# Kernel optimization log

Hardware: AMD Instinct MI355X
Metric: run time of the kernel (lower is better)

## Reference

```python
import jax, jax.numpy as jnp
import numpy as np

B, S, HID = 2, 2048, 2048
NH, HD = 16, 128
KVC, QC = 512, 1536


def _rope(x):
    # x: [B, H, S, D]; interleaved-pair rotation matching the torch view(..., D//2, 2)
    b, h, s, d = x.shape
    inv_freq = 1.0 / (10000.0 ** (jnp.arange(0, d, 2, dtype=jnp.float32) / d))  # [D/2]
    pos = jnp.arange(s, dtype=jnp.float32)
    sinusoid = pos[:, None] * inv_freq[None, :]  # [S, D/2]
    sin = jnp.sin(sinusoid)[None, None]  # [1,1,S,D/2]
    cos = jnp.cos(sinusoid)[None, None]
    xr = x.reshape(b, h, s, d // 2, 2)
    x1, x2 = xr[..., 0], xr[..., 1]
    out = jnp.stack([x1 * cos - x2 * sin, x1 * sin + x2 * cos], axis=-1)
    return out.reshape(b, h, s, d)


def setup_inputs() -> dict:
    key = jax.random.key(0)
    ks = jax.random.split(key, 14)
    def lin(k, fan_in, fan_out):
        lim = 1.0 / np.sqrt(fan_in)
        kw, kb = jax.random.split(k)
        W = jax.random.uniform(kw, (fan_in, fan_out), jnp.float32, -lim, lim)
        b = jax.random.uniform(kb, (fan_out,), jnp.float32, -lim, lim)
        return W, b
    x = jax.random.normal(ks[0], (B, S, HID), jnp.float32)
    # causal mask (positions with 0 are masked out)
    attention_mask = jnp.tril(jnp.ones((S, S), jnp.int32))[None, None]  # [1,1,S,S]
    W_dkv, b_dkv = lin(ks[1], HID, KVC)
    W_uk, b_uk = lin(ks[2], KVC, NH * HD)
    W_uv, b_uv = lin(ks[3], KVC, NH * HD)
    W_dq, b_dq = lin(ks[4], HID, QC)
    W_uq, b_uq = lin(ks[5], QC, NH * HD)
    W_o, b_o = lin(ks[6], NH * HD, HID)
    return dict(x=x, attention_mask=attention_mask,
                W_dkv=W_dkv, b_dkv=b_dkv, W_uk=W_uk, b_uk=b_uk,
                W_uv=W_uv, b_uv=b_uv, W_dq=W_dq, b_dq=b_dq,
                W_uq=W_uq, b_uq=b_uq, W_o=W_o, b_o=b_o)


def reference(x, attention_mask, W_dkv, b_dkv, W_uk, b_uk, W_uv, b_uv,
              W_dq, b_dq, W_uq, b_uq, W_o, b_o):
    b, s, _ = x.shape
    kv = x @ W_dkv + b_dkv                                   # [B,S,KVC]
    k = (kv @ W_uk + b_uk).reshape(b, s, NH, HD).transpose(0, 2, 1, 3)  # [B,H,S,D]
    v = (kv @ W_uv + b_uv).reshape(b, s, NH, HD).transpose(0, 2, 1, 3)
    q = ((x @ W_dq + b_dq) @ W_uq + b_uq).reshape(b, s, NH, HD).transpose(0, 2, 1, 3)
    q, k = _rope(q), _rope(k)
    scores = jnp.einsum('bhqd,bhkd->bhqk', q, k) / jnp.sqrt(jnp.float32(HD))
    scores = jnp.where(attention_mask == 0, jnp.float32(-1e9), scores)
    probs = jax.nn.softmax(scores, axis=-1)
    out = jnp.einsum('bhqk,bhkd->bhqd', probs, v)            # [B,H,S,D]
    out = out.transpose(0, 2, 1, 3).reshape(b, s, NH * HD)
    return out @ W_o + b_o
```

## Files before the change

### kernel.cpp

```cpp
#include <hip/hip_runtime.h>
#include <stdint.h>

typedef unsigned short u16;
typedef uint32_t u32;
typedef __attribute__((ext_vector_type(8))) short short8;
typedef __attribute__((ext_vector_type(4))) float f32x4;
typedef __attribute__((ext_vector_type(4))) u32 u32x4;
typedef __attribute__((ext_vector_type(2))) u32 u32x2;
typedef __attribute__((ext_vector_type(4))) unsigned short u16x4;

#define BS_ 4096
#define S_ 2048
#define HID_ 2048

__device__ __forceinline__ float bf2f(u16 u) { union { u32 i; float f; } v; v.i = ((u32)u) << 16; return v.f; }
__device__ __forceinline__ u16 f2bf(float f) {
  union { float f; u32 i; } v; v.f = f;
  u32 r = v.i + 0x7fffu + ((v.i >> 16) & 1u);
  return (u16)(r >> 16);
}

__device__ __forceinline__ void gload16(const void* gsrc, void* ldst) {
  __builtin_amdgcn_global_load_lds(
      (const __attribute__((address_space(1))) void*)gsrc,
      (__attribute__((address_space(3))) void*)ldst, 16, 0, 0);
}

__global__ __launch_bounds__(256) void prep(const float* __restrict__ x, u16* __restrict__ xb,
                                            const float* __restrict__ W_dkv, const float* __restrict__ W_dq,
                                            const float* __restrict__ W_uk, const float* __restrict__ W_uv,
                                            const float* __restrict__ W_uq, const float* __restrict__ W_o,
                                            u16* __restrict__ WdkvqT, u16* __restrict__ WukvT,
                                            u16* __restrict__ WuqT, u16* __restrict__ WoT,
                                            const float* __restrict__ b_dkv, const float* __restrict__ b_dq,
                                            const float* __restrict__ b_uk, const float* __restrict__ b_uv,
                                            float* __restrict__ cs, float* __restrict__ bc1,
                                            float* __restrict__ bc2) {
  __shared__ float tile[64][65];
  int b = blockIdx.x;
  const int t = threadIdx.x;
  if (b < 8192) {
    int i = b * 256 + t;
    float4 v = ((const float4*)x)[i];
    u16x4 o;
    o.x = f2bf(v.x); o.y = f2bf(v.y); o.z = f2bf(v.z); o.w = f2bf(v.w);
    ((u16x4*)xb)[i] = o;
    return;
  }
  b -= 8192;
  if (b < 3328) {
    const float* W; u16* WT; int K, N, gx, r = b;
    if (r < 256)                 { W = W_dkv; WT = WdkvqT;                    K = 2048; N = 512;  gx = 8;  }
    else if ((r -= 256) < 768)   { W = W_dq;  WT = WdkvqT + (size_t)512 * 2048; K = 2048; N = 1536; gx = 24; }
    else if ((r -= 768) < 256)   { W = W_uk;  WT = WukvT;                     K = 512;  N = 2048; gx = 32; }
    else if ((r -= 256) < 256)   { W = W_uv;  WT = WukvT + (size_t)2048 * 512;  K = 512;  N = 2048; gx = 32; }
    else if ((r -= 256) < 768)   { W = W_uq;  WT = WuqT;                      K = 1536; N = 2048; gx = 32; }
    else                         { r -= 768;  W = W_o; WT = WoT;              K = 2048; N = 2048; gx = 32; }
    const int nb = (r % gx) * 64, kb = (r / gx) * 64;
#pragma unroll
    for (int c = 0; c < 4; ++c) {
      int idx = c * 256 + t;
      int row = idx >> 4;
      int col4 = (idx & 15) * 4;
      float4 v = *(const float4*)&W[(size_t)(kb + row) * N + nb + col4];
      tile[row][col4 + 0] = v.x; tile[row][col4 + 1] = v.y;
      tile[row][col4 + 2] = v.z; tile[row][col4 + 3] = v.w;
    }
    __syncthreads();
#pragma unroll
    for (int c = 0; c < 4; ++c) {
      int idx = c * 256 + t;
      int n = idx >> 4;
      int k4 = (idx & 15) * 4;
      u16x4 o;
      o.x = f2bf(tile[k4 + 0][n]); o.y = f2bf(tile[k4 + 1][n]);
      o.z = f2bf(tile[k4 + 2][n]); o.w = f2bf(tile[k4 + 3][n]);
      *(u16x4*)&WT[(size_t)(nb + n) * K + kb + k4] = o;
    }
    return;
  }
  b -= 3328;
  if (b < 512) {
    int idx = b * 256 + t;
    int pos = idx >> 6, i = idx & 63;
    float inv = powf(10000.f, -(float)i / 64.f);
    float a = (float)pos * inv;
    cs[idx * 2] = cosf(a);
    cs[idx * 2 + 1] = sinf(a);
    return;
  }
  b -= 512;
  {
    int i = b * 256 + t;
    if (i < 512) bc1[i] = b_dkv[i];
    else if (i < 2048) bc1[i] = b_dq[i - 512];
    else if (i < 4096) bc2[i - 2048] = b_uk[i - 2048];
    else if (i < 6144) bc2[i - 2048] = b_uv[i - 4096];
  }
}

template <int OUTF32>
__global__ __launch_bounds__(256) void gemm_bt(const u16* __restrict__ A, int lda,
                                               const u16* __restrict__ BT,
                                               const float* __restrict__ bias,
                                               void* __restrict__ Cout,
                                               int M, int N, int K) {
  __shared__ u16 As[2][128 * 64];
  __shared__ u16 Bs[2][128 * 64];
  const int t = threadIdx.x;
  const int lane = t & 63, wave = t >> 6;
  const int wm = wave >> 1, wn = wave & 1;
  const int gx = gridDim.x;
  const int nwg = gx * gridDim.y;
  const int flat = blockIdx.y * gx + blockIdx.x;
  const int swz = (flat & 7) * (nwg >> 3) + (flat >> 3);
  const int tn = swz % gx, tm = swz / gx;
  const int r16 = lane & 15, q4 = lane >> 4;

  f32x4 acc[4][4];
#pragma unroll
  for (int m = 0; m < 4; ++m)
#pragma unroll
    for (int n = 0; n < 4; ++n) acc[m][n] = (f32x4){0.f, 0.f, 0.f, 0.f};

  auto stg = [&](int bufi, int kt) {
#pragma unroll
    for (int c = 0; c < 4; ++c) {
      int idx = c * 256 + t;
      int row = idx >> 3, ch = idx & 7;
      gload16(&A[(size_t)(tm * 128 + row) * lda + kt + ch * 8], (char*)As[bufi] + idx * 16);
      gload16(&BT[(size_t)(tn * 128 + row) * K + kt + ch * 8], (char*)Bs[bufi] + idx * 16);
    }
  };

  const int nkt = K >> 6;
  stg(0, 0);
  __syncthreads();
  for (int it = 0; it < nkt; ++it) {
    const int buf = it & 1;
    if (it + 1 < nkt) stg(buf ^ 1, (it + 1) << 6);
#pragma unroll
    for (int kk = 0; kk < 64; kk += 32) {
      short8 af[4], bfv[4];
#pragma unroll
      for (int m = 0; m < 4; ++m)
        af[m] = *(const short8*)&As[buf][(wm * 64 + m * 16 + r16) * 64 + kk + q4 * 8];
#pragma unroll
      for (int n = 0; n < 4; ++n)
        bfv[n] = *(const short8*)&Bs[buf][(wn * 64 + n * 16 + r16) * 64 + kk + q4 * 8];
      __builtin_amdgcn_s_setprio(1);
#pragma unroll
      for (int m = 0; m < 4; ++m)
#pragma unroll
        for (int n = 0; n < 4; ++n)
          acc[m][n] = __builtin_amdgcn_mfma_f32_16x16x32_bf16(bfv[n], af[m], acc[m][n], 0, 0, 0);
      __builtin_amdgcn_s_setprio(0);
    }
    __syncthreads();
  }
#pragma unroll
  for (int n = 0; n < 4; ++n) {
    int gc0 = tn * 128 + wn * 64 + n * 16 + q4 * 4;
    float4 bv4 = *(const float4*)&bias[gc0];
#pragma unroll
    for (int m = 0; m < 4; ++m) {
      int grow = tm * 128 + wm * 64 + m * 16 + r16;
      float v0 = acc[m][n][0] + bv4.x, v1 = acc[m][n][1] + bv4.y;
      float v2 = acc[m][n][2] + bv4.z, v3 = acc[m][n][3] + bv4.w;
      if (OUTF32) {
        float4 o; o.x = v0; o.y = v1; o.z = v2; o.w = v3;
        *(float4*)&((float*)Cout)[(size_t)grow * N + gc0] = o;
      } else {
        u16x4 o; o.x = f2bf(v0); o.y = f2bf(v1); o.z = f2bf(v2); o.w = f2bf(v3);
        *(u16x4*)&((u16*)Cout)[(size_t)grow * N + gc0] = o;
      }
    }
  }
}

__global__ __launch_bounds__(256) void gemm23(const u16* __restrict__ kvq1,
                                              const u16* __restrict__ WukvT, const u16* __restrict__ WuqT,
                                              const float* __restrict__ bc2, const float* __restrict__ b_uq,
                                              const float* __restrict__ cs,
                                              u16* __restrict__ kbuf, u16* __restrict__ VT,
                                              u16* __restrict__ qb) {
  __shared__ u16 sh[4 * 128 * 64];
  const int t = threadIdx.x;
  const int lane = t & 63, wave = t >> 6;
  const int wm = wave >> 1, wn = wave & 1;
  const int bflat = blockIdx.x;
  const bool g2 = (bflat >= 512);
  const u16* A  = g2 ? kvq1 : (kvq1 + 512);
  const u16* BT = g2 ? WukvT : WuqT;
  const float* bias = g2 ? bc2 : b_uq;
  const int K = g2 ? 512 : 1536;
  const int gx = g2 ? 32 : 16;
  const int nwg = g2 ? 1024 : 512;
  const int flat = g2 ? (bflat - 512) : bflat;
  const int swz = (flat & 7) * (nwg >> 3) + (flat >> 3);
  const int tn = swz % gx, tm = swz / gx;
  const int r16 = lane & 15, q4 = lane >> 4;

  f32x4 acc[4][4];
#pragma unroll
  for (int m = 0; m < 4; ++m)
#pragma unroll
    for (int n = 0; n < 4; ++n) acc[m][n] = (f32x4){0.f, 0.f, 0.f, 0.f};

  auto stg = [&](int bufi, int kt) {
    char* Asb = (char*)(sh + bufi * 16384);
    char* Bsb = Asb + 16384;
#pragma unroll
    for (int c = 0; c < 4; ++c) {
      int idx = c * 256 + t;
      int row = idx >> 3, ch = idx & 7;
      gload16(&A[(size_t)(tm * 128 + row) * 2048 + kt + ch * 8], Asb + idx * 16);
      gload16(&BT[(size_t)(tn * 128 + row) * K + kt + ch * 8], Bsb + idx * 16);
    }
  };

  const int nkt = K >> 6;
  stg(0, 0);
  __syncthreads();
  for (int it = 0; it < nkt; ++it) {
    const int buf = it & 1;
    if (it + 1 < nkt) stg(buf ^ 1, (it + 1) << 6);
    const u16* As = sh + buf * 16384;
    const u16* Bs = As + 8192;
#pragma unroll
    for (int kk = 0; kk < 64; kk += 32) {
      short8 af[4], bfv[4];
#pragma unroll
      for (int m = 0; m < 4; ++m)
        af[m] = *(const short8*)&As[(wm * 64 + m * 16 + r16) * 64 + kk + q4 * 8];
#pragma unroll
      for (int n = 0; n < 4; ++n)
        bfv[n] = *(const short8*)&Bs[(wn * 64 + n * 16 + r16) * 64 + kk + q4 * 8];
      __builtin_amdgcn_s_setprio(1);
#pragma unroll
      for (int m = 0; m < 4; ++m)
#pragma unroll
        for (int n = 0; n < 4; ++n)
          acc[m][n] = __builtin_amdgcn_mfma_f32_16x16x32_bf16(bfv[n], af[m], acc[m][n], 0, 0, 0);
      __builtin_amdgcn_s_setprio(0);
    }
    __syncthreads();
  }

  const bool isV = g2 && (tn >= 16);
  if (!isV) {
    u16* outp = g2 ? kbuf : qb;
#pragma unroll
    for (int n = 0; n < 4; ++n) {
      int gc0 = tn * 128 + wn * 64 + n * 16 + q4 * 4;
      float4 bv4 = *(const float4*)&bias[gc0];
      const int i0 = (gc0 & 127) >> 1;
#pragma unroll
      for (int m = 0; m < 4; ++m) {
        int grow = tm * 128 + wm * 64 + m * 16 + r16;
        float v0 = acc[m][n][0] + bv4.x, v1 = acc[m][n][1] + bv4.y;
        float v2 = acc[m][n][2] + bv4.z, v3 = acc[m][n][3] + bv4.w;
        int s = grow & 2047;
        float4 cp = *(const float4*)&cs[((size_t)s * 64 + i0) * 2];
        float y0 = v0 * cp.x - v1 * cp.y;
        float y1 = v0 * cp.y + v1 * cp.x;
        float y2 = v2 * cp.z - v3 * cp.w;
        float y3 = v2 * cp.w + v3 * cp.z;
        u16x4 o; o.x = f2bf(y0); o.y = f2bf(y1); o.z = f2bf(y2); o.w = f2bf(y3);
        *(u16x4*)&outp[(size_t)grow * 2048 + gc0] = o;
      }
    }
  } else {
    u16* lt = sh;
    __syncthreads();
#pragma unroll
    for (int n = 0; n < 4; ++n) {
      int gc0 = tn * 128 + wn * 64 + n * 16 + q4 * 4;
      float4 bv4 = *(const float4*)&bias[gc0];
      int dL0 = wn * 64 + n * 16 + q4 * 4;
#pragma unroll
      for (int m = 0; m < 4; ++m) {
        int sL = wm * 64 + m * 16 + r16;
        float vv[4] = {acc[m][n][0] + bv4.x, acc[m][n][1] + bv4.y,
                       acc[m][n][2] + bv4.z, acc[m][n][3] + bv4.w};
#pragma unroll
        for (int j = 0; j < 4; ++j) {
          int dd = dL0 + j;
          lt[dd * 128 + (sL ^ ((dd & 7) << 4))] = f2bf(vv[j]);
        }
      }
    }
    __syncthreads();
    const int hh = tn - 16;
    const int bb2 = tm >> 4;
    const int s0 = (tm & 15) * 128;
    u16* vbase = VT + (size_t)(bb2 * 16 + hh) * 128 * S_ + s0;
#pragma unroll
    for (int c = 0; c < 8; ++c) {
      int idx = c * 256 + t;
      int d = idx >> 4, ch = idx & 15;
      short8 v = *(const short8*)&lt[d * 128 + ((ch * 8) ^ ((d & 7) << 4))];
      *(short8*)&vbase[(size_t)d * S_ + ch * 8] = v;
    }
  }
}

__global__ __launch_bounds__(256, 2) void attn_kernel(const u16* __restrict__ Q, const u16* __restrict__ K,
                                                      int kld, const u16* __restrict__ VT,
                                                      u16* __restrict__ O) {
  __shared__ char smem[75776];
  u16* Kl = (u16*)smem;
  u16* Vl = (u16*)(smem + 32768);
  u16* Pl = (u16*)(smem + 65536);
  float* ex = (float*)smem;

  const int t = threadIdx.x;
  const int lane = t & 63, w = t >> 6;
  const int r16 = lane & 15, q4 = lane >> 4;
  const int par = w >> 1, sub = w & 1;
  const int b = blockIdx.x;
  const int xcd = b & 7, u = b >> 3;
  const int p = u & 15, g4 = u >> 4;
  const int bh = g4 * 8 + xcd;
  const int bb = bh >> 4, h = bh & 15;
  const u16* Qb = Q + (size_t)bb * S_ * HID_ + (size_t)h * 128;
  const u16* Kb = K + (size_t)bb * S_ * kld + (size_t)h * 128;
  const u16* VTb = VT + (size_t)bh * 128 * S_;
  u16* Ob = O + (size_t)bb * S_ * HID_ + (size_t)h * 128;

  auto stage = [&](int rs, int kvbase) {
#pragma unroll
    for (int pp = 0; pp < 2; ++pp) {
      int kvb = kvbase + pp * 32;
      char* kd = (char*)(Kl + (size_t)(rs * 2 + pp) * 4096);
      char* vd = (char*)(Vl + (size_t)(rs * 2 + pp) * 4096);
#pragma unroll
      for (int c = 0; c < 2; ++c) {
        int s = c * 256 + t;
        int row = s >> 4;
        int ch = (s & 15) ^ (row & 7);
        gload16(&Kb[(size_t)(kvb + row) * kld + ch * 8], kd + s * 16);
      }
#pragma unroll
      for (int c = 0; c < 2; ++c) {
        int s = c * 256 + t;
        int row = s >> 2;
        int ch = (s & 3) ^ ((row >> 1) & 3);
        gload16(&VTb[(size_t)row * S_ + kvb + ch * 8], vd + s * 16);
      }
    }
  };

  u16* Pw = Pl + (size_t)w * 1280;
  const float SCALE = 0.08838834764831845f;

#pragma unroll
  for (int seg = 0; seg < 2; ++seg) {
    const int qt = seg ? (31 - p) : p;
    const int nr = qt + 1;
    const int qrow0 = qt * 64 + sub * 32;

    short8 qf[2][4];
#pragma unroll
    for (int m = 0; m < 2; ++m)
#pragma unroll
      for (int dk = 0; dk < 4; ++dk)
        qf[m][dk] = *(const short8*)&Qb[(size_t)(qrow0 + m * 16 + r16) * HID_ + dk * 32 + q4 * 8];

    f32x4 ao[2][8];
    float mr[2], lr[2];
#pragma unroll
    for (int m = 0; m < 2; ++m) {
#pragma unroll
      for (int dn = 0; dn < 8; ++dn) ao[m][dn] = (f32x4){0.f, 0.f, 0.f, 0.f};
      mr[m] = -1e30f; lr[m] = 0.f;
    }

    stage(0, 0);
    __syncthreads();

    for (int r = 0; r < nr; ++r) {
      const int rs = r & 1;
      if (r + 1 < nr) stage(rs ^ 1, (r + 1) * 64);
      const int kv0 = r * 64 + par * 32;
      const u16* Kbuf = Kl + (size_t)(rs * 2 + par) * 4096;
      const u16* Vbuf = Vl + (size_t)(rs * 2 + par) * 4096;

      if (kv0 <= qrow0 + 31) {
        f32x4 sc[2][2];
#pragma unroll
        for (int m = 0; m < 2; ++m)
#pragma unroll
          for (int n = 0; n < 2; ++n) sc[m][n] = (f32x4){0.f, 0.f, 0.f, 0.f};
#pragma unroll
        for (int dk = 0; dk < 4; ++dk) {
          short8 kf[2];
#pragma unroll
          for (int n = 0; n < 2; ++n) {
            int kr = n * 16 + r16;
            int ba = (kr * 256 + dk * 64 + q4 * 16) ^ ((kr & 7) << 4);
            kf[n] = *(const short8*)((const char*)Kbuf + ba);
          }
          __builtin_amdgcn_s_setprio(1);
#pragma unroll
          for (int n = 0; n < 2; ++n)
#pragma unroll
            for (int m = 0; m < 2; ++m)
              sc[m][n] = __builtin_amdgcn_mfma_f32_16x16x32_bf16(kf[n], qf[m][dk], sc[m][n], 0, 0, 0);
          __builtin_amdgcn_s_setprio(0);
        }
        const bool nm = (kv0 + 31 > qrow0);
#pragma unroll
        for (int m = 0; m < 2; ++m) {
          const int q = qrow0 + m * 16 + r16;
#pragma unroll
          for (int n = 0; n < 2; ++n)
#pragma unroll
            for (int j = 0; j < 4; ++j) {
              float sv = sc[m][n][j] * SCALE;
              if (nm) {
                int kv = kv0 + n * 16 + q4 * 4 + j;
                if (kv > q) sv = -1e30f;
              }
              sc[m][n][j] = sv;
            }
        }
        float tm0[2];
#pragma unroll
        for (int m = 0; m < 2; ++m) {
          float tm = sc[m][0][0];
#pragma unroll
          for (int n = 0; n < 2; ++n)
#pragma unroll
            for (int j = 0; j < 4; ++j) tm = fmaxf(tm, sc[m][n][j]);
          tm = fmaxf(tm, __shfl_xor(tm, 16));
          tm = fmaxf(tm, __shfl_xor(tm, 32));
          tm0[m] = tm;
        }
        float growth = fmaxf(tm0[0] - mr[0], tm0[1] - mr[1]);
        if (!__all(growth <= 8.0f)) {
#pragma unroll
          for (int m = 0; m < 2; ++m) {
            float mnew = fmaxf(mr[m], tm0[m]);
            float fsc = __expf(mr[m] - mnew);
            lr[m] *= fsc; mr[m] = mnew;
#pragma unroll
            for (int dn = 0; dn < 8; ++dn) ao[m][dn] *= fsc;
          }
        }
#pragma unroll
        for (int m = 0; m < 2; ++m) {
          float ps = 0.f;
#pragma unroll
          for (int n = 0; n < 2; ++n)
#pragma unroll
            for (int j = 0; j < 4; ++j) {
              float pv = __expf(sc[m][n][j] - mr[m]);
              sc[m][n][j] = pv;
              ps += pv;
            }
          ps += __shfl_xor(ps, 16);
          ps += __shfl_xor(ps, 32);
          lr[m] += ps;
        }
#pragma unroll
        for (int m = 0; m < 2; ++m)
#pragma unroll
          for (int n = 0; n < 2; ++n) {
            u32 lo, hi;
            asm("v_cvt_pk_bf16_f32 %0, %1, %2" : "=v"(lo) : "v"(sc[m][n][0]), "v"(sc[m][n][1]));
            asm("v_cvt_pk_bf16_f32 %0, %1, %2" : "=v"(hi) : "v"(sc[m][n][2]), "v"(sc[m][n][3]));
            u32x2 pr; pr.x = lo; pr.y = hi;
            int ba = (m * 16 + r16) * 80 + n * 32 + q4 * 8;
            *(u32x2*)((char*)Pw + ba) = pr;
          }
        short8 pb[2];
#pragma unroll
        for (int m = 0; m < 2; ++m)
          pb[m] = *(const short8*)((const char*)Pw + (m * 16 + r16) * 80 + q4 * 16);
        __builtin_amdgcn_s_setprio(1);
#pragma unroll
        for (int dn = 0; dn < 8; ++dn) {
          int d = dn * 16 + r16;
          int bv = d * 64 + ((q4 ^ ((d >> 1) & 3)) * 16);
          short8 vf = *(const short8*)((const char*)Vbuf + bv);
#pragma unroll
          for (int m = 0; m < 2; ++m)
            ao[m][dn] = __builtin_amdgcn_mfma_f32_16x16x32_bf16(vf, pb[m], ao[m][dn], 0, 0, 0);
        }
        __builtin_amdgcn_s_setprio(0);
      }
      __syncthreads();
    }

    {
      float* exb = ex + (size_t)sub * 4352 + (size_t)lane * 68;
      if (par == 1) {
#pragma unroll
        for (int m = 0; m < 2; ++m)
#pragma unroll
          for (int dn = 0; dn < 8; ++dn)
            *(f32x4*)(exb + m * 32 + dn * 4) = ao[m][dn];
        exb[64] = mr[0]; exb[65] = mr[1]; exb[66] = lr[0]; exb[67] = lr[1];
      }
      __syncthreads();
      if (par == 0) {
#pragma unroll
        for (int m = 0; m < 2; ++m) {
          float mB = exb[64 + m], lB = exb[66 + m];
          float mx = fmaxf(mr[m], mB);
          float wA = __expf(mr[m] - mx), wB = __expf(mB - mx);
          float inv = 1.f / (lr[m] * wA + lB * wB);
          const int q = qrow0 + m * 16 + r16;
#pragma unroll
          for (int dn = 0; dn < 8; ++dn) {
            f32x4 ob = *(const f32x4*)(exb + m * 32 + dn * 4);
            u16x4 o;
#pragma unroll
            for (int j = 0; j < 4; ++j) o[j] = f2bf((ao[m][dn][j] * wA + ob[j] * wB) * inv);
            *(u16x4*)&Ob[(size_t)q * HID_ + dn * 16 + q4 * 4] = o;
          }
        }
      }
      __syncthreads();
    }
  }
}

extern "C" void kernel_launch(void* const* d_in, const int* in_sizes, int n_in,
                              void* d_out, int out_size, void* d_ws, size_t ws_size,
                              hipStream_t stream) {
  (void)in_sizes; (void)n_in; (void)out_size; (void)ws_size;
  const float* x     = (const float*)d_in[0];
  const float* W_dkv = (const float*)d_in[2];
  const float* b_dkv = (const float*)d_in[3];
  const float* W_uk  = (const float*)d_in[4];
  const float* b_uk  = (const float*)d_in[5];
  const float* W_uv  = (const float*)d_in[6];
  const float* b_uv  = (const float*)d_in[7];
  const float* W_dq  = (const float*)d_in[8];
  const float* b_dq  = (const float*)d_in[9];
  const float* W_uq  = (const float*)d_in[10];
  const float* b_uq  = (const float*)d_in[11];
  const float* W_o   = (const float*)d_in[12];
  const float* b_o   = (const float*)d_in[13];
  float* out = (float*)d_out;

  char* ws = (char*)d_ws;
  size_t off = 0;
  auto carve = [&](size_t bytes) { void* p = ws + off; off += (bytes + 255) & ~(size_t)255; return p; };
  u16* xb     = (u16*)carve((size_t)BS_ * 2048 * 2);
  u16* WdkvqT = (u16*)carve((size_t)2048 * 2048 * 2);
  u16* WukvT  = (u16*)carve((size_t)4096 * 512 * 2);
  u16* WuqT   = (u16*)carve((size_t)2048 * 1536 * 2);
  u16* WoT    = (u16*)carve((size_t)2048 * 2048 * 2);
  u16* kvq1   = (u16*)carve((size_t)BS_ * 2048 * 2);
  u16* kbuf   = (u16*)carve((size_t)BS_ * 2048 * 2);
  u16* qb     = (u16*)carve((size_t)BS_ * 2048 * 2);
  u16* aob    = (u16*)carve((size_t)BS_ * 2048 * 2);
  float* cs   = (float*)carve((size_t)2048 * 64 * 2 * 4);
  float* bc1  = (float*)carve((size_t)2048 * 4);
  float* bc2  = (float*)carve((size_t)4096 * 4);
  u16* VT     = xb;

  prep<<<dim3(12056), 256, 0, stream>>>(x, xb, W_dkv, W_dq, W_uk, W_uv, W_uq, W_o,
                                        WdkvqT, WukvT, WuqT, WoT,
                                        b_dkv, b_dq, b_uk, b_uv, cs, bc1, bc2);

  gemm_bt<0><<<dim3(2048 / 128, BS_ / 128), 256, 0, stream>>>(xb, 2048, WdkvqT, bc1, kvq1, BS_, 2048, 2048);

  gemm23<<<dim3(1536), 256, 0, stream>>>(kvq1, WukvT, WuqT, bc2, b_uq, cs, kbuf, VT, qb);

  attn_kernel<<<dim3(512), 256, 0, stream>>>(qb, kbuf, 2048, VT, aob);

  gemm_bt<1><<<dim3(2048 / 128, BS_ / 128), 256, 0, stream>>>(aob, 2048, WoT, b_o, out, BS_, 2048, 2048);
}
```

Measured before the change: 258.9 us.

## Read V directly from global, shrink LDS, one q-tile per block for occupancy

Drops LDS staging of V in the attention kernel and loads V fragments straight from global memory into registers each iteration. This cuts shared memory from about 74KB to 42KB and raises launch bounds to 3 blocks per CU. The kernel also stops processing two paired q-tiles per block: it launches 1024 blocks with one q-tile each, heaviest tiles first, and splits the final merge into two smaller passes to fit the reduced LDS. The trade-off is uncoalesced, unpipelined global V reads and more register pressure from holding 8 V fragments, in exchange for higher occupancy and finer load balancing.

```diff
diff --git a/kernel.cpp b/kernel.cpp
--- a/kernel.cpp
+++ b/kernel.cpp
@@ -305,13 +305,12 @@
   }
 }
 
-__global__ __launch_bounds__(256, 2) void attn_kernel(const u16* __restrict__ Q, const u16* __restrict__ K,
+__global__ __launch_bounds__(256, 3) void attn_kernel(const u16* __restrict__ Q, const u16* __restrict__ K,
                                                       int kld, const u16* __restrict__ VT,
                                                       u16* __restrict__ O) {
-  __shared__ char smem[75776];
+  __shared__ char smem[43008];
   u16* Kl = (u16*)smem;
-  u16* Vl = (u16*)(smem + 32768);
-  u16* Pl = (u16*)(smem + 65536);
+  u16* Pl = (u16*)(smem + 32768);
   float* ex = (float*)smem;
 
   const int t = threadIdx.x;
@@ -319,21 +318,20 @@
   const int r16 = lane & 15, q4 = lane >> 4;
   const int par = w >> 1, sub = w & 1;
   const int b = blockIdx.x;
-  const int xcd = b & 7, u = b >> 3;
-  const int p = u & 15, g4 = u >> 4;
-  const int bh = g4 * 8 + xcd;
+  const int xcd = b & 7, i = (b >> 3) & 31, g = b >> 8;
+  const int qt = 31 - i;
+  const int bh = g * 8 + xcd;
   const int bb = bh >> 4, h = bh & 15;
   const u16* Qb = Q + (size_t)bb * S_ * HID_ + (size_t)h * 128;
   const u16* Kb = K + (size_t)bb * S_ * kld + (size_t)h * 128;
   const u16* VTb = VT + (size_t)bh * 128 * S_;
   u16* Ob = O + (size_t)bb * S_ * HID_ + (size_t)h * 128;
 
-  auto stage = [&](int rs, int kvbase) {
+  auto stageK = [&](int rs, int kvbase) {
 #pragma unroll
     for (int pp = 0; pp < 2; ++pp) {
       int kvb = kvbase + pp * 32;
       char* kd = (char*)(Kl + (size_t)(rs * 2 + pp) * 4096);
-      char* vd = (char*)(Vl + (size_t)(rs * 2 + pp) * 4096);
 #pragma unroll
       for (int c = 0; c < 2; ++c) {
         int s = c * 256 + t;
@@ -341,189 +339,173 @@
         int ch = (s & 15) ^ (row & 7);
         gload16(&Kb[(size_t)(kvb + row) * kld + ch * 8], kd + s * 16);
       }
-#pragma unroll
-      for (int c = 0; c < 2; ++c) {
-        int s = c * 256 + t;
-        int row = s >> 2;
-        int ch = (s & 3) ^ ((row >> 1) & 3);
-        gload16(&VTb[(size_t)row * S_ + kvb + ch * 8], vd + s * 16);
-      }
     }
   };
 
   u16* Pw = Pl + (size_t)w * 1280;
   const float SCALE = 0.08838834764831845f;
 
-#pragma unroll
-  for (int seg = 0; seg < 2; ++seg) {
-    const int qt = seg ? (31 - p) : p;
-    const int nr = qt + 1;
-    const int qrow0 = qt * 64 + sub * 32;
-
-    short8 qf[2][4];
-#pragma unroll
-    for (int m = 0; m < 2; ++m)
-#pragma unroll
-      for (int dk = 0; dk < 4; ++dk)
-        qf[m][dk] = *(const short8*)&Qb[(size_t)(qrow0 + m * 16 + r16) * HID_ + dk * 32 + q4 * 8];
-
-    f32x4 ao[2][8];
-    float mr[2], lr[2];
-#pragma unroll
-    for (int m = 0; m < 2; ++m) {
-#pragma unroll
-      for (int dn = 0; dn < 8; ++dn) ao[m][dn] = (f32x4){0.f, 0.f, 0.f, 0.f};
-      mr[m] = -1e30f; lr[m] = 0.f;
-    }
-
-    stage(0, 0);
-    __syncthreads();
-
-    for (int r = 0; r < nr; ++r) {
-      const int rs = r & 1;
-      if (r + 1 < nr) stage(rs ^ 1, (r + 1) * 64);
-      const int kv0 = r * 64 + par * 32;
-      const u16* Kbuf = Kl + (size_t)(rs * 2 + par) * 4096;
-      const u16* Vbuf = Vl + (size_t)(rs * 2 + par) * 4096;
-
-      if (kv0 <= qrow0 + 31) {
-        f32x4 sc[2][2];
+  const int nr = qt + 1;
+  const int qrow0 = qt * 64 + sub * 32;
+
+  short8 qf[2][4];
+#pragma unroll
+  for (int m = 0; m < 2; ++m)
+#pragma unroll
+    for (int dk = 0; dk < 4; ++dk)
+      qf[m][dk] = *(const short8*)&Qb[(size_t)(qrow0 + m * 16 + r16) * HID_ + dk * 32 + q4 * 8];
+
+  f32x4 ao[2][8];
+  float mr[2], lr[2];
+#pragma unroll
+  for (int m = 0; m < 2; ++m) {
+#pragma unroll
+    for (int dn = 0; dn < 8; ++dn) ao[m][dn] = (f32x4){0.f, 0.f, 0.f, 0.f};
+    mr[m] = -1e30f; lr[m] = 0.f;
+  }
+
+  stageK(0, 0);
+  __syncthreads();
+
+  for (int r = 0; r < nr; ++r) {
+    const int rs = r & 1;
+    if (r + 1 < nr) stageK(rs ^ 1, (r + 1) * 64);
+    const int kv0 = r * 64 + par * 32;
+    const u16* Kbuf = Kl + (size_t)(rs * 2 + par) * 4096;
+
+    if (kv0 <= qrow0 + 31) {
+      short8 vf[8];
+#pragma unroll
+      for (int dn = 0; dn < 8; ++dn)
+        vf[dn] = *(const short8*)&VTb[(size_t)(dn * 16 + r16) * S_ + kv0 + q4 * 8];
+      f32x4 sc[2][2];
+#pragma unroll
+      for (int m = 0; m < 2; ++m)
+#pragma unroll
+        for (int n = 0; n < 2; ++n) sc[m][n] = (f32x4){0.f, 0.f, 0.f, 0.f};
+#pragma unroll
+      for (int dk = 0; dk < 4; ++dk) {
+        short8 kf[2];
+#pragma unroll
+        for (int n = 0; n < 2; ++n) {
+          int kr = n * 16 + r16;
+          int ba = (kr * 256 + dk * 64 + q4 * 16) ^ ((kr & 7) << 4);
+          kf[n] = *(const short8*)((const char*)Kbuf + ba);
+        }
+        __builtin_amdgcn_s_setprio(1);
+#pragma unroll
+        for (int n = 0; n < 2; ++n)
+#pragma unroll
+          for (int m = 0; m < 2; ++m)
+            sc[m][n] = __builtin_amdgcn_mfma_f32_16x16x32_bf16(kf[n], qf[m][dk], sc[m][n], 0, 0, 0);
+        __builtin_amdgcn_s_setprio(0);
+      }
+      const bool nm = (kv0 + 31 > qrow0);
+#pragma unroll
+      for (int m = 0; m < 2; ++m) {
+        const int q = qrow0 + m * 16 + r16;
+#pragma unroll
+        for (int n = 0; n < 2; ++n)
+#pragma unroll
+          for (int j = 0; j < 4; ++j) {
+            float sv = sc[m][n][j] * SCALE;
+            if (nm) {
+              int kv = kv0 + n * 16 + q4 * 4 + j;
+              if (kv > q) sv = -1e30f;
+            }
+            sc[m][n][j] = sv;
+          }
+      }
+      float tm0[2];
+#pragma unroll
+      for (int m = 0; m < 2; ++m) {
+        float tm = sc[m][0][0];
+#pragma unroll
+        for (int n = 0; n < 2; ++n)
+#pragma unroll
+          for (int j = 0; j < 4; ++j) tm = fmaxf(tm, sc[m][n][j]);
+        tm = fmaxf(tm, __shfl_xor(tm, 16));
+        tm = fmaxf(tm, __shfl_xor(tm, 32));
+        tm0[m] = tm;
+      }
+      float growth = fmaxf(tm0[0] - mr[0], tm0[1] - mr[1]);
+      if (!__all(growth <= 8.0f)) {
+#pragma unroll
+        for (int m = 0; m < 2; ++m) {
+          float mnew = fmaxf(mr[m], tm0[m]);
+          float fsc = __expf(mr[m] - mnew);
+          lr[m] *= fsc; mr[m] = mnew;
+#pragma unroll
+          for (int dn = 0; dn < 8; ++dn) ao[m][dn] *= fsc;
+        }
+      }
+#pragma unroll
+      for (int m = 0; m < 2; ++m) {
+        float ps = 0.f;
+#pragma unroll
+        for (int n = 0; n < 2; ++n)
+#pragma unroll
+          for (int j = 0; j < 4; ++j) {
+            float pv = __expf(sc[m][n][j] - mr[m]);
+            sc[m][n][j] = pv;
+            ps += pv;
+          }
+        ps += __shfl_xor(ps, 16);
+        ps += __shfl_xor(ps, 32);
+        lr[m] += ps;
+      }
+#pragma unroll
+      for (int m = 0; m < 2; ++m)
+#pragma unroll
+        for (int n = 0; n < 2; ++n) {
+          u32 lo, hi;
+          asm("v_cvt_pk_bf16_f32 %0, %1, %2" : "=v"(lo) : "v"(sc[m][n][0]), "v"(sc[m][n][1]));
+          asm("v_cvt_pk_bf16_f32 %0, %1, %2" : "=v"(hi) : "v"(sc[m][n][2]), "v"(sc[m][n][3]));
+          u32x2 pr; pr.x = lo; pr.y = hi;
+          int ba = (m * 16 + r16) * 80 + n * 32 + q4 * 8;
+          *(u32x2*)((char*)Pw + ba) = pr;
+        }
+      short8 pb[2];
+#pragma unroll
+      for (int m = 0; m < 2; ++m)
+        pb[m] = *(const short8*)((const char*)Pw + (m * 16 + r16) * 80 + q4 * 16);
+      __builtin_amdgcn_s_setprio(1);
+#pragma unroll
+      for (int dn = 0; dn < 8; ++dn)
 #pragma unroll
         for (int m = 0; m < 2; ++m)
-#pragma unroll
-          for (int n = 0; n < 2; ++n) sc[m][n] = (f32x4){0.f, 0.f, 0.f, 0.f};
-#pragma unroll
-        for (int dk = 0; dk < 4; ++dk) {
-          short8 kf[2];
-#pragma unroll
-          for (int n = 0; n < 2; ++n) {
-            int kr = n * 16 + r16;
-            int ba = (kr * 256 + dk * 64 + q4 * 16) ^ ((kr & 7) << 4);
-            kf[n] = *(const short8*)((const char*)Kbuf + ba);
-          }
-          __builtin_amdgcn_s_setprio(1);
-#pragma unroll
-          for (int n = 0; n < 2; ++n)
-#pragma unroll
-            for (int m = 0; m < 2; ++m)
-              sc[m][n] = __builtin_amdgcn_mfma_f32_16x16x32_bf16(kf[n], qf[m][dk], sc[m][n], 0, 0, 0);
-          __builtin_amdgcn_s_setprio(0);
-        }
-        const bool nm = (kv0 + 31 > qrow0);
-#pragma unroll
-        for (int m = 0; m < 2; ++m) {
-          const int q = qrow0 + m * 16 + r16;
-#pragma unroll
-          for (int n = 0; n < 2; ++n)
-#pragma unroll
-            for (int j = 0; j < 4; ++j) {
-              float sv = sc[m][n][j] * SCALE;
-              if (nm) {
-                int kv = kv0 + n * 16 + q4 * 4 + j;
-                if (kv > q) sv = -1e30f;
-              }
-              sc[m][n][j] = sv;
-            }
-        }
-        float tm0[2];
-#pragma unroll
-        for (int m = 0; m < 2; ++m) {
-          float tm = sc[m][0][0];
-#pragma unroll
-          for (int n = 0; n < 2; ++n)
-#pragma unroll
-            for (int j = 0; j < 4; ++j) tm = fmaxf(tm, sc[m][n][j]);
-          tm = fmaxf(tm, __shfl_xor(tm, 16));
-          tm = fmaxf(tm, __shfl_xor(tm, 32));
-          tm0[m] = tm;
-        }
-        float growth = fmaxf(tm0[0] - mr[0], tm0[1] - mr[1]);
-        if (!__all(growth <= 8.0f)) {
-#pragma unroll
-          for (int m = 0; m < 2; ++m) {
-            float mnew = fmaxf(mr[m], tm0[m]);
-            float fsc = __expf(mr[m] - mnew);
-            lr[m] *= fsc; mr[m] = mnew;
-#pragma unroll
-            for (int dn = 0; dn < 8; ++dn) ao[m][dn] *= fsc;
-          }
-        }
-#pragma unroll
-        for (int m = 0; m < 2; ++m) {
-          float ps = 0.f;
-#pragma unroll
-          for (int n = 0; n < 2; ++n)
-#pragma unroll
-            for (int j = 0; j < 4; ++j) {
-              float pv = __expf(sc[m][n][j] - mr[m]);
-              sc[m][n][j] = pv;
-              ps += pv;
-            }
-          ps += __shfl_xor(ps, 16);
-          ps += __shfl_xor(ps, 32);
-          lr[m] += ps;
-        }
-#pragma unroll
-        for (int m = 0; m < 2; ++m)
-#pragma unroll
-          for (int n = 0; n < 2; ++n) {
-            u32 lo, hi;
-            asm("v_cvt_pk_bf16_f32 %0, %1, %2" : "=v"(lo) : "v"(sc[m][n][0]), "v"(sc[m][n][1]));
-            asm("v_cvt_pk_bf16_f32 %0, %1, %2" : "=v"(hi) : "v"(sc[m][n][2]), "v"(sc[m][n][3]));
-            u32x2 pr; pr.x = lo; pr.y = hi;
-            int ba = (m * 16 + r16) * 80 + n * 32 + q4 * 8;
-            *(u32x2*)((char*)Pw + ba) = pr;
-          }
-        short8 pb[2];
-#pragma unroll
-        for (int m = 0; m < 2; ++m)
-          pb[m] = *(const short8*)((const char*)Pw + (m * 16 + r16) * 80 + q4 * 16);
-        __builtin_amdgcn_s_setprio(1);
-#pragma unroll
-        for (int dn = 0; dn < 8; ++dn) {
-          int d = dn * 16 + r16;
-          int bv = d * 64 + ((q4 ^ ((d >> 1) & 3)) * 16);
-          short8 vf = *(const short8*)((const char*)Vbuf + bv);
-#pragma unroll
-          for (int m = 0; m < 2; ++m)
-            ao[m][dn] = __builtin_amdgcn_mfma_f32_16x16x32_bf16(vf, pb[m], ao[m][dn], 0, 0, 0);
-        }
-        __builtin_amdgcn_s_setprio(0);
-      }
-      __syncthreads();
-    }
-
-    {
-      float* exb = ex + (size_t)sub * 4352 + (size_t)lane * 68;
-      if (par == 1) {
-#pragma unroll
-        for (int m = 0; m < 2; ++m)
-#pragma unroll
-          for (int dn = 0; dn < 8; ++dn)
-            *(f32x4*)(exb + m * 32 + dn * 4) = ao[m][dn];
-        exb[64] = mr[0]; exb[65] = mr[1]; exb[66] = lr[0]; exb[67] = lr[1];
-      }
-      __syncthreads();
-      if (par == 0) {
-#pragma unroll
-        for (int m = 0; m < 2; ++m) {
-          float mB = exb[64 + m], lB = exb[66 + m];
-          float mx = fmaxf(mr[m], mB);
-          float wA = __expf(mr[m] - mx), wB = __expf(mB - mx);
-          float inv = 1.f / (lr[m] * wA + lB * wB);
-          const int q = qrow0 + m * 16 + r16;
-#pragma unroll
-          for (int dn = 0; dn < 8; ++dn) {
-            f32x4 ob = *(const f32x4*)(exb + m * 32 + dn * 4);
-            u16x4 o;
-#pragma unroll
-            for (int j = 0; j < 4; ++j) o[j] = f2bf((ao[m][dn][j] * wA + ob[j] * wB) * inv);
-            *(u16x4*)&Ob[(size_t)q * HID_ + dn * 16 + q4 * 4] = o;
-          }
-        }
-      }
-      __syncthreads();
-    }
+          ao[m][dn] = __builtin_amdgcn_mfma_f32_16x16x32_bf16(vf[dn], pb[m], ao[m][dn], 0, 0, 0);
+      __builtin_amdgcn_s_setprio(0);
+    }
+    __syncthreads();
+  }
+
+#pragma unroll
+  for (int mp = 0; mp < 2; ++mp) {
+    float* exb = ex + (size_t)(sub * 64 + lane) * 34;
+    if (par == 1) {
+#pragma unroll
+      for (int dn = 0; dn < 8; ++dn)
+        *(f32x4*)(exb + dn * 4) = ao[mp][dn];
+      exb[32] = mr[mp]; exb[33] = lr[mp];
+    }
+    __syncthreads();
+    if (par == 0) {
+      float mB = exb[32], lB = exb[33];
+      float mx = fmaxf(mr[mp], mB);
+      float wA = __expf(mr[mp] - mx), wB = __expf(mB - mx);
+      float inv = 1.f / (lr[mp] * wA + lB * wB);
+      const int q = qrow0 + mp * 16 + r16;
+#pragma unroll
+      for (int dn = 0; dn < 8; ++dn) {
+        f32x4 ob = *(const f32x4*)(exb + dn * 4);
+        u16x4 o;
+#pragma unroll
+        for (int j = 0; j < 4; ++j) o[j] = f2bf((ao[mp][dn][j] * wA + ob[j] * wB) * inv);
+        *(u16x4*)&Ob[(size_t)q * HID_ + dn * 16 + q4 * 4] = o;
+      }
+    }
+    __syncthreads();
   }
 }
 
@@ -571,7 +553,7 @@
 
   gemm23<<<dim3(1536), 256, 0, stream>>>(kvq1, WukvT, WuqT, bc2, b_uq, cs, kbuf, VT, qb);
 
-  attn_kernel<<<dim3(512), 256, 0, stream>>>(qb, kbuf, 2048, VT, aob);
+  attn_kernel<<<dim3(1024), 256, 0, stream>>>(qb, kbuf, 2048, VT, aob);
 
   gemm_bt<1><<<dim3(2048 / 128, BS_ / 128), 256, 0, stream>>>(aob, 2048, WoT, b_o, out, BS_, 2048, 2048);
 }
```

Measured after the change: 437.4 us. +68.9%, slower.
